# Performance work log

Hardware: AMD Instinct MI355X
Metric: run time of the kernel (lower is better)

## Reference

```python
import jax, jax.numpy as jnp
import numpy as np

N = 8192          # number of signals (rows of Y)
DIM_BASIS = 512   # signal dimension n
NUM_BASIS = 2048  # dictionary atoms m (overcomplete)
SC_ITERS = 20     # FISTA iterations
PM_ITERS = 100    # power-method iterations


def setup_inputs() -> dict:
    key = jax.random.key(0)
    kY, kW = jax.random.split(key)
    Y = jax.random.normal(kY, (N, DIM_BASIS), jnp.float32)
    W = jax.random.normal(kW, (DIM_BASIS, NUM_BASIS), jnp.float32)
    # NormDict applied in __init__: unit-norm columns
    W = W / jnp.linalg.norm(W, axis=0, keepdims=True)
    K = jnp.asarray(0.1, jnp.float32)  # lamda for FISTA soft-threshold
    return {"Y": Y, "W": W, "K": K}


def _soft(x, lam):
    return jnp.sign(x) * jax.nn.relu(jnp.abs(x) - lam)


def _power_method(W):
    # largest eigenvalue of W^T W (W: [n, m]); fixed random init for determinism
    X0 = jax.random.normal(jax.random.key(1), (1, W.shape[1]), W.dtype)

    def body(i, carry):
        X, _ = carry
        X = (X @ W.T) @ W          # X <- X W^T W, shape [1, m]
        nm = jnp.linalg.norm(X)
        return (X / nm, nm)

    _, nm = jax.lax.fori_loop(0, PM_ITERS, body, (X0, jnp.asarray(1.0, W.dtype)))
    return nm


def _fista(Y, W, lam, iters):
    c = _power_method(W)
    eta = 1.0 / c
    Gamma0 = _soft(Y @ (eta * W), lam)     # [N, m]
    Yn = jnp.linalg.norm(Y)

    def step(carry, _):
        Gamma, Z, t = carry
        residual = Z @ W.T - Y                              # [N, n]
        Gamma_new = _soft(Z - eta * (residual @ W), lam / c)
        t_new = (1.0 + jnp.sqrt(1.0 + 4.0 * t * t)) / 2.0
        Z_new = Gamma_new + ((t - 1.0) / t_new) * (Gamma_new - Gamma)
        nrm = jnp.linalg.norm(residual) / Yn
        return (Gamma_new, Z_new, t_new), nrm

    init = (Gamma0, Gamma0, jnp.asarray(1.0, Y.dtype))
    (Gamma, _, _), norms = jax.lax.scan(step, init, None, length=iters)
    return Gamma, norms


def reference(Y, W, K):
    # NormDict at start of forward (done on .data in torch -> no grad through norm)
    Wn = W / jax.lax.stop_gradient(jnp.linalg.norm(W, axis=0, keepdims=True))
    # W.requires_grad_(False) during sparse coding
    W_ng = jax.lax.stop_gradient(Wn)
    Gamma, norms = _fista(Y, W_ng, K, SC_ITERS)
    X = Gamma @ Wn.T   # reconstruction, grad flows to W here only
    return X, Gamma, norms
```

## Files before the change

### kernel.cpp

```cpp
#include <hip/hip_runtime.h>
#include <cmath>

#define NR   8192
#define DB   512
#define NB   2048
#define ITERS 20
#define NSQ   9

typedef _Float16 hfrag_t __attribute__((ext_vector_type(8)));
typedef __attribute__((ext_vector_type(4))) float accv_t;
typedef unsigned short us4 __attribute__((ext_vector_type(4)));
typedef unsigned short us8 __attribute__((ext_vector_type(8)));
typedef float f4 __attribute__((ext_vector_type(4)));

#define SL_Y2   0
#define SL_NUM  1
#define SL_DEN  2
#define SL_C    3
#define SL_ETA  4
#define SL_THR  5
#define SL_TR   6
#define SL_RES2 16

__device__ inline unsigned short f2h(float f) {
  _Float16 h = (_Float16)f;
  return __builtin_bit_cast(unsigned short, h);
}
__device__ inline float h2f(unsigned short u) {
  _Float16 h = __builtin_bit_cast(_Float16, u);
  return (float)h;
}
__device__ inline float softthr(float x, float t) {
  float a = fabsf(x) - t;
  return a > 0.f ? copysignf(a, x) : 0.f;
}


template<int MI, int NI, int NKT>
__device__ inline void gemm_tt(const unsigned short* __restrict__ At, int NTka,
                               const unsigned short* __restrict__ Bt, int NTkb,
                               int mt0, int nt0, accv_t acc[MI][NI]) {
  const int lane = threadIdx.x & 63;
  const int l16 = lane & 15, quad = lane >> 4;
  const int off = l16 * 16 + (quad & 1) * 8;
  const int kh = quad >> 1;
#pragma unroll
  for (int mi = 0; mi < MI; ++mi)
#pragma unroll
    for (int ni = 0; ni < NI; ++ni) acc[mi][ni] = (accv_t){0.f, 0.f, 0.f, 0.f};

#pragma unroll 4
  for (int kt = 0; kt < NKT; ++kt) {
    const int ktile = (kt << 1) + kh;
    hfrag_t af[MI], bf[NI];
#pragma unroll
    for (int mi = 0; mi < MI; ++mi)
      af[mi] = *(const hfrag_t*)&At[(((size_t)(mt0 + mi) * NTka + ktile) << 8) + off];
#pragma unroll
    for (int ni = 0; ni < NI; ++ni)
      bf[ni] = *(const hfrag_t*)&Bt[(((size_t)(nt0 + ni) * NTkb + ktile) << 8) + off];
#pragma unroll
    for (int mi = 0; mi < MI; ++mi)
#pragma unroll
      for (int ni = 0; ni < NI; ++ni)
        acc[mi][ni] = __builtin_amdgcn_mfma_f32_16x16x32_f16(bf[ni], af[mi], acc[mi][ni], 0, 0, 0);
  }
}

__device__ inline size_t ctile_off(int mt, int nt, int NTn) {
  int lane = threadIdx.x & 63;
  return (((size_t)mt * NTn + nt) << 8) + (lane & 15) * 16 + (lane >> 4) * 4;
}

__global__ void k_zero(float* slots, float* colsq) {
  if (threadIdx.x < 64) slots[threadIdx.x] = 0.f;
  for (int i = threadIdx.x; i < NB; i += 256) colsq[i] = 0.f;
}

__global__ void k_colsq(const float* __restrict__ W, float* __restrict__ colsq) {
  int j = blockIdx.x * 256 + threadIdx.x;
  int r0 = blockIdx.y * 64;
  float s = 0.f;
  for (int i = 0; i < 64; ++i) { float v = W[(size_t)(r0 + i) * NB + j]; s += v * v; }
  atomicAdd(&colsq[j], s);
}

__global__ void k_wnorm(const float* __restrict__ W, const float* __restrict__ colsq,
                        unsigned short* __restrict__ Wn_t, unsigned short* __restrict__ Wt_t) {
  int tx = threadIdx.x & 31, ty = threadIdx.x >> 5;
  int j = blockIdx.x * 32 + tx;
  float inv = 1.0f / sqrtf(colsq[j]);
#pragma unroll
  for (int r = 0; r < 4; ++r) {
    int i = blockIdx.y * 32 + ty + r * 8;
    unsigned short h = f2h(W[(size_t)i * NB + j] * inv);
    Wn_t[(((size_t)(i >> 4) * (NB / 16) + (j >> 4)) << 8) + (i & 15) * 16 + (j & 15)] = h;
    Wt_t[(((size_t)(j >> 4) * (DB / 16) + (i >> 4)) << 8) + (j & 15) * 16 + (i & 15)] = h;
  }
}

__global__ __launch_bounds__(256) void k_ynorm(const float* __restrict__ Y,
                                               unsigned short* __restrict__ Yh,
                                               float* __restrict__ slots) {
  __shared__ float part[4];
  int w = threadIdx.x >> 6, lane = threadIdx.x & 63;
  float s = 0.f;
#pragma unroll
  for (int rr = 0; rr < 4; ++rr) {
    int m = blockIdx.x * 16 + w * 4 + rr;
    const float* yrow = &Y[(size_t)m * DB + lane * 8];
    f4 v0 = *(const f4*)yrow;
    f4 v1 = *(const f4*)(yrow + 4);
    us8 h;
#pragma unroll
    for (int q = 0; q < 4; ++q) {
      h[q] = f2h(v0[q]);     s += v0[q] * v0[q];
      h[4 + q] = f2h(v1[q]); s += v1[q] * v1[q];
    }
    *(us8*)&Yh[(((size_t)(m >> 4) * 32 + (lane >> 1)) << 8) + (m & 15) * 16 + (lane & 1) * 8] = h;
  }
  for (int off = 32; off > 0; off >>= 1) s += __shfl_xor(s, off);
  if (lane == 0) part[w] = s;
  __syncthreads();
  if (threadIdx.x == 0) atomicAdd(&slots[SL_Y2], part[0] + part[1] + part[2] + part[3]);
}

__global__ __launch_bounds__(256) void k_sq(const float* __restrict__ S, float* __restrict__ D,
                                            const float* __restrict__ trIn, float* __restrict__ trOut) {
  __shared__ float tA[32][33], tB[32][33];
  int tx = threadIdx.x & 31, ty = threadIdx.x >> 5;
  int r0 = blockIdx.y * 32, c0 = blockIdx.x * 32;
  float inv = 1.0f / trIn[0];
  float acc[4] = {0.f, 0.f, 0.f, 0.f};
  for (int kt = 0; kt < 16; ++kt) {
    __syncthreads();
#pragma unroll
    for (int r = 0; r < 4; ++r) {
      tA[ty + r * 8][tx] = S[(size_t)(r0 + ty + r * 8) * DB + kt * 32 + tx];
      tB[ty + r * 8][tx] = S[(size_t)(kt * 32 + ty + r * 8) * DB + c0 + tx];
    }
    __syncthreads();
#pragma unroll
    for (int kk = 0; kk < 32; ++kk) {
      float b = tB[kk][tx];
#pragma unroll
      for (int r = 0; r < 4; ++r) acc[r] += tA[ty + r * 8][kk] * b;
    }
  }
  float inv2 = inv * inv;
#pragma unroll
  for (int r = 0; r < 4; ++r) {
    int row = r0 + ty + r * 8, col = c0 + tx;
    float v = acc[r] * inv2;
    D[(size_t)row * DB + col] = v;
    if (row == col) atomicAdd(trOut, v);
  }
}

__global__ void k_rayleigh(const float* __restrict__ Bm, const float* __restrict__ S,
                           float* __restrict__ slots) {
  int tid = blockIdx.x * 256 + threadIdx.x;
  float num = 0.f, den = 0.f;
  for (int i = tid; i < DB * DB; i += 256 * 256) {
    float s = S[i];
    num += Bm[i] * s;
    if ((i >> 9) == (i & 511)) den += s;
  }
  for (int off = 32; off > 0; off >>= 1) { num += __shfl_xor(num, off); den += __shfl_xor(den, off); }
  if ((threadIdx.x & 63) == 0) { atomicAdd(&slots[SL_NUM], num); atomicAdd(&slots[SL_DEN], den); }
}

__global__ void k_derive(float* slots, const float* __restrict__ Kp) {
  if (threadIdx.x == 0) {
    float cc = slots[SL_NUM] / slots[SL_DEN];
    slots[SL_C] = cc;
    float eta = 1.0f / cc;
    slots[SL_ETA] = eta;
    slots[SL_THR] = Kp[0] * eta;
  }
}

__global__ void k_norms(const float* __restrict__ slots, float* __restrict__ out) {
  int i = threadIdx.x;
  if (i < ITERS) out[i] = sqrtf(slots[SL_RES2 + i] / slots[SL_Y2]);
}

__global__ __launch_bounds__(512) void k_gemm_bbuild(const unsigned short* __restrict__ Wn_t,
                                                     float* __restrict__ Bm, float* __restrict__ slots) {
  __shared__ float red[4][64][33];
  accv_t acc[2][4];
  int w = threadIdx.x >> 6, lane = threadIdx.x & 63;
  int wk = w >> 2, wm = w & 3;
  int mt0 = blockIdx.y * 8 + wm * 2, nt0 = blockIdx.x * 4;
  const size_t koff = (size_t)wk * 64 * 256;
  gemm_tt<2, 4, NB / 64>(Wn_t + koff, NB / 16, Wn_t + koff, NB / 16, mt0, nt0, acc);
  if (wk == 1) {
#pragma unroll
    for (int mi = 0; mi < 2; ++mi)
#pragma unroll
      for (int ni = 0; ni < 4; ++ni)
#pragma unroll
        for (int r = 0; r < 4; ++r)
          red[wm][lane][mi * 16 + ni * 4 + r] = acc[mi][ni][r];
  }
  __syncthreads();
  if (wk == 0) {
    int l16 = lane & 15, quad = lane >> 4;
    float tr = 0.f;
#pragma unroll
    for (int mi = 0; mi < 2; ++mi)
#pragma unroll
      for (int ni = 0; ni < 4; ++ni) {
        int m = (mt0 + mi) * 16 + l16, nb = (nt0 + ni) * 16 + quad * 4;
        f4 o;
#pragma unroll
        for (int r = 0; r < 4; ++r) {
          o[r] = acc[mi][ni][r] + red[wm][lane][mi * 16 + ni * 4 + r];
          if (m == nb + r) tr += o[r];
        }
        *(f4*)&Bm[(size_t)m * DB + nb] = o;
      }
    if (tr != 0.f) atomicAdd(&slots[SL_TR], tr);
  }
}

__global__ __launch_bounds__(256) void k_gemm_init(const unsigned short* __restrict__ Yh,
                                                   const unsigned short* __restrict__ Wt_t,
                                                   const float* __restrict__ slots,
                                                   const float* __restrict__ Kp,
                                                   unsigned short* __restrict__ Gh,
                                                   unsigned short* __restrict__ Zh) {
  accv_t acc[4][4];
  int w = threadIdx.x >> 6;
  int h = blockIdx.x;
  int xcd = h & 7, slot = h >> 3;
  int band = xcd * 8 + (slot >> 4);
  int nt = slot & 15;
  int mt0 = band * 8 + (w >> 1) * 4, nt0 = nt * 8 + (w & 1) * 4;
  gemm_tt<4, 4, DB / 32>(Yh, DB / 16, Wt_t, DB / 16, mt0, nt0, acc);
  float eta = slots[SL_ETA], lam = Kp[0];
#pragma unroll
  for (int mi = 0; mi < 4; ++mi)
#pragma unroll
    for (int ni = 0; ni < 4; ++ni) {
      size_t tb = ctile_off(mt0 + mi, nt0 + ni, NB / 16);
      us4 gq;
#pragma unroll
      for (int r = 0; r < 4; ++r) gq[r] = f2h(softthr(acc[mi][ni][r] * eta, lam));
      *(us4*)&Gh[tb] = gq;
      *(us4*)&Zh[tb] = gq;
    }
}

__global__ __launch_bounds__(512) void k_gemm_res(const unsigned short* __restrict__ Zh,
                                                  const unsigned short* __restrict__ Wn_t,
                                                  const unsigned short* __restrict__ Yh,
                                                  unsigned short* __restrict__ Rh,
                                                  float* __restrict__ res2slot) {
  __shared__ float red[4][64][65];
  accv_t acc[4][4];
  int w = threadIdx.x >> 6, lane = threadIdx.x & 63;
  int wk = w >> 2, wm = w & 3;
  int h = blockIdx.x;
  int xcd = h & 7, slot = h >> 3;
  int band = xcd * 4 + (slot >> 3);
  int nt = slot & 7;
  int mt0 = band * 16 + wm * 4, nt0 = nt * 4;
  const size_t koff = (size_t)wk * 64 * 256;
  gemm_tt<4, 4, NB / 64>(Zh + koff, NB / 16, Wn_t + koff, NB / 16, mt0, nt0, acc);
  if (wk == 1) {
#pragma unroll
    for (int mi = 0; mi < 4; ++mi)
#pragma unroll
      for (int ni = 0; ni < 4; ++ni)
#pragma unroll
        for (int r = 0; r < 4; ++r)
          red[wm][lane][mi * 16 + ni * 4 + r] = acc[mi][ni][r];
  }
  __syncthreads();
  if (wk == 0) {
    float s2 = 0.f;
#pragma unroll
    for (int mi = 0; mi < 4; ++mi)
#pragma unroll
      for (int ni = 0; ni < 4; ++ni) {
        size_t tb = ctile_off(mt0 + mi, nt0 + ni, DB / 16);
        us4 yq = *(const us4*)&Yh[tb];
        us4 rq;
#pragma unroll
        for (int r = 0; r < 4; ++r) {
          float rv = acc[mi][ni][r] + red[wm][lane][mi * 16 + ni * 4 + r] - h2f(yq[r]);
          rq[r] = f2h(rv);
          s2 += rv * rv;
        }
        *(us4*)&Rh[tb] = rq;
      }
    for (int off = 32; off > 0; off >>= 1) s2 += __shfl_xor(s2, off);
    if (lane == 0) atomicAdd(res2slot, s2);
  }
}

__global__ __launch_bounds__(256) void k_gemm_upd(const unsigned short* __restrict__ Rh,
                                                  const unsigned short* __restrict__ Wt_t,
                                                  const float* __restrict__ slots,
                                                  unsigned short* __restrict__ Gh,
                                                  unsigned short* __restrict__ Zh,
                                                  float* __restrict__ GammaOut,
                                                  float mom, int writeFinal) {
  accv_t acc[4][4];
  int w = threadIdx.x >> 6, lane = threadIdx.x & 63;
  int h = blockIdx.x;
  int xcd = h & 7, slot = h >> 3;
  int band = xcd * 8 + (slot >> 4);
  int nt = slot & 15;
  int mt0 = band * 8 + (w >> 1) * 4, nt0 = nt * 8 + (w & 1) * 4;
  gemm_tt<4, 4, DB / 32>(Rh, DB / 16, Wt_t, DB / 16, mt0, nt0, acc);
  int l16 = lane & 15, quad = lane >> 4;
  float eta = slots[SL_ETA], thr = slots[SL_THR];
#pragma unroll
  for (int mi = 0; mi < 4; ++mi)
#pragma unroll
    for (int ni = 0; ni < 4; ++ni) {
      size_t tb = ctile_off(mt0 + mi, nt0 + ni, NB / 16);
      us4 zq = *(const us4*)&Zh[tb];
      us4 gq = *(const us4*)&Gh[tb];
      us4 gho, zho;
      f4 gf;
#pragma unroll
      for (int r = 0; r < 4; ++r) {
        float z = h2f(zq[r]);
        float gold = h2f(gq[r]);
        float gn = softthr(z - eta * acc[mi][ni][r], thr);
        float zn = gn + mom * (gn - gold);
        gho[r] = f2h(gn);
        zho[r] = f2h(zn);
        gf[r] = gn;
      }
      *(us4*)&Gh[tb] = gho;
      *(us4*)&Zh[tb] = zho;
      if (writeFinal) {
        int m = (mt0 + mi) * 16 + l16, nb = (nt0 + ni) * 16 + quad * 4;
        *(f4*)&GammaOut[(size_t)m * NB + nb] = gf;
      }
    }
}

__global__ __launch_bounds__(512) void k_gemm_x(const unsigned short* __restrict__ Gh,
                                                const unsigned short* __restrict__ Wn_t,
                                                float* __restrict__ X) {
  __shared__ float red[4][64][65];
  accv_t acc[4][4];
  int w = threadIdx.x >> 6, lane = threadIdx.x & 63;
  int wk = w >> 2, wm = w & 3;
  int h = blockIdx.x;
  int xcd = h & 7, slot = h >> 3;
  int band = xcd * 4 + (slot >> 3);
  int nt = slot & 7;
  int mt0 = band * 16 + wm * 4, nt0 = nt * 4;
  const size_t koff = (size_t)wk * 64 * 256;
  gemm_tt<4, 4, NB / 64>(Gh + koff, NB / 16, Wn_t + koff, NB / 16, mt0, nt0, acc);
  if (wk == 1) {
#pragma unroll
    for (int mi = 0; mi < 4; ++mi)
#pragma unroll
      for (int ni = 0; ni < 4; ++ni)
#pragma unroll
        for (int r = 0; r < 4; ++r)
          red[wm][lane][mi * 16 + ni * 4 + r] = acc[mi][ni][r];
  }
  __syncthreads();
  if (wk == 0) {
    int l16 = lane & 15, quad = lane >> 4;
#pragma unroll
    for (int mi = 0; mi < 4; ++mi)
#pragma unroll
      for (int ni = 0; ni < 4; ++ni) {
        int m = (mt0 + mi) * 16 + l16, nb = (nt0 + ni) * 16 + quad * 4;
        f4 o;
#pragma unroll
        for (int r = 0; r < 4; ++r)
          o[r] = acc[mi][ni][r] + red[wm][lane][mi * 16 + ni * 4 + r];
        *(f4*)&X[(size_t)m * DB + nb] = o;
      }
  }
}

extern "C" void kernel_launch(void* const* d_in, const int* in_sizes, int n_in,
                              void* d_out, int out_size, void* d_ws, size_t ws_size,
                              hipStream_t stream) {
  const float* Y  = (const float*)d_in[0];
  const float* W  = (const float*)d_in[1];
  const float* Kp = (const float*)d_in[2];

  float* Xout     = (float*)d_out;
  float* GammaOut = Xout + (size_t)NR * DB;
  float* NormsOut = GammaOut + (size_t)NR * NB;

  char* p = (char*)d_ws;
  auto carve = [&](size_t bytes) -> void* {
    void* r = (void*)p; p += (bytes + 255) & ~(size_t)255; return r;
  };
  float* slots = (float*)carve(64 * 4);
  float* colsq = (float*)carve(NB * 4);
  float* Bmat  = (float*)carve((size_t)DB * DB * 4);
  float* S0    = (float*)carve((size_t)DB * DB * 4);
  float* S1    = (float*)carve((size_t)DB * DB * 4);
  unsigned short* Wn_t = (unsigned short*)carve((size_t)DB * NB * 2);
  unsigned short* Wt_t = (unsigned short*)carve((size_t)NB * DB * 2);
  unsigned short* Yh   = (unsigned short*)carve((size_t)NR * DB * 2);
  unsigned short* Rh   = (unsigned short*)carve((size_t)NR * DB * 2);
  unsigned short* Zh   = (unsigned short*)carve((size_t)NR * NB * 2);
  unsigned short* Gh   = (unsigned short*)carve((size_t)NR * NB * 2);

  k_zero<<<1, 256, 0, stream>>>(slots, colsq);
  k_colsq<<<dim3(NB / 256, DB / 64), 256, 0, stream>>>(W, colsq);
  k_wnorm<<<dim3(NB / 32, DB / 32), 256, 0, stream>>>(W, colsq, Wn_t, Wt_t);
  k_ynorm<<<512, 256, 0, stream>>>(Y, Yh, slots);

  k_gemm_bbuild<<<dim3(DB / 64, DB / 128), 512, 0, stream>>>(Wn_t, Bmat, slots);
  float* ss[2] = {S0, S1};
  for (int k = 0; k < NSQ; ++k) {
    const float* in = (k == 0) ? Bmat : ss[(k + 1) & 1];
    k_sq<<<dim3(16, 16), 256, 0, stream>>>(in, ss[k & 1], slots + SL_TR + k, slots + SL_TR + k + 1);
  }
  k_rayleigh<<<256, 256, 0, stream>>>(Bmat, ss[(NSQ + 1) & 1], slots);
  k_derive<<<1, 64, 0, stream>>>(slots, Kp);

  k_gemm_init<<<1024, 256, 0, stream>>>(Yh, Wt_t, slots, Kp, Gh, Zh);
  double t = 1.0;
  for (int i = 0; i < ITERS; ++i) {
    k_gemm_res<<<256, 512, 0, stream>>>(Zh, Wn_t, Yh, Rh, slots + SL_RES2 + i);
    double tn = (1.0 + sqrt(1.0 + 4.0 * t * t)) / 2.0;
    float mom = (float)((t - 1.0) / tn);
    t = tn;
    k_gemm_upd<<<1024, 256, 0, stream>>>(Rh, Wt_t, slots, Gh, Zh, GammaOut,
                                         mom, (i == ITERS - 1) ? 1 : 0);
  }
  k_gemm_x<<<256, 512, 0, stream>>>(Gh, Wn_t, Xout);
  k_norms<<<1, 64, 0, stream>>>(slots, NormsOut);
}
```

Baseline: 2.148 ms.

## Split K across warp pairs in update GEMM with LDS reduction

The update GEMM (residual times W) now uses 512-thread blocks in which two groups of four warps each compute half of the K dimension for the same output tiles. The partial sums are exchanged through shared memory, and each warp finishes half of the M sub-tiles in the soft-threshold epilogue. Block tiling also changes, so each block covers a 16x4 tile region instead of 8x8. The aim is to double the number of waves working on each output and halve the serial K loop per warp, at the cost of an LDS reduction and a block-wide sync. Separately, the last iteration no longer writes Z, since it is not used after the loop.

```diff
diff --git a/kernel.cpp b/kernel.cpp
--- a/kernel.cpp
+++ b/kernel.cpp
@@ -300,46 +300,65 @@
   }
 }
 
-__global__ __launch_bounds__(256) void k_gemm_upd(const unsigned short* __restrict__ Rh,
+__global__ __launch_bounds__(512) void k_gemm_upd(const unsigned short* __restrict__ Rh,
                                                   const unsigned short* __restrict__ Wt_t,
                                                   const float* __restrict__ slots,
                                                   unsigned short* __restrict__ Gh,
                                                   unsigned short* __restrict__ Zh,
                                                   float* __restrict__ GammaOut,
                                                   float mom, int writeFinal) {
+  __shared__ float red[8][64][33];
   accv_t acc[4][4];
   int w = threadIdx.x >> 6, lane = threadIdx.x & 63;
+  int wk = w >> 2, wm = w & 3;
   int h = blockIdx.x;
   int xcd = h & 7, slot = h >> 3;
-  int band = xcd * 8 + (slot >> 4);
-  int nt = slot & 15;
-  int mt0 = band * 8 + (w >> 1) * 4, nt0 = nt * 8 + (w & 1) * 4;
-  gemm_tt<4, 4, DB / 32>(Rh, DB / 16, Wt_t, DB / 16, mt0, nt0, acc);
+  int band = xcd * 4 + (slot >> 5);
+  int nt = slot & 31;
+  int mt0 = band * 16 + wm * 4, nt0 = nt * 4;
+  const size_t koff = (size_t)wk * 16 * 256;
+  gemm_tt<4, 4, DB / 64>(Rh + koff, DB / 16, Wt_t + koff, DB / 16, mt0, nt0, acc);
+  {
+    int mbase = wk ? 0 : 2;
+#pragma unroll
+    for (int mi = 0; mi < 2; ++mi)
+#pragma unroll
+      for (int ni = 0; ni < 4; ++ni)
+#pragma unroll
+        for (int r = 0; r < 4; ++r)
+          red[w][lane][mi * 16 + ni * 4 + r] = acc[mbase + mi][ni][r];
+  }
+  __syncthreads();
+  const int fbase = wk ? 2 : 0;
+  const int pw = w ^ 4;
   int l16 = lane & 15, quad = lane >> 4;
   float eta = slots[SL_ETA], thr = slots[SL_THR];
 #pragma unroll
-  for (int mi = 0; mi < 4; ++mi)
+  for (int mi = 0; mi < 2; ++mi)
 #pragma unroll
     for (int ni = 0; ni < 4; ++ni) {
-      size_t tb = ctile_off(mt0 + mi, nt0 + ni, NB / 16);
+      int mt = fbase + mi;
+      size_t tb = ctile_off(mt0 + mt, nt0 + ni, NB / 16);
       us4 zq = *(const us4*)&Zh[tb];
       us4 gq = *(const us4*)&Gh[tb];
       us4 gho, zho;
       f4 gf;
 #pragma unroll
       for (int r = 0; r < 4; ++r) {
+        float g = acc[mt][ni][r] + red[pw][lane][mi * 16 + ni * 4 + r];
         float z = h2f(zq[r]);
         float gold = h2f(gq[r]);
-        float gn = softthr(z - eta * acc[mi][ni][r], thr);
+        float gn = softthr(z - eta * g, thr);
         float zn = gn + mom * (gn - gold);
         gho[r] = f2h(gn);
         zho[r] = f2h(zn);
         gf[r] = gn;
       }
       *(us4*)&Gh[tb] = gho;
-      *(us4*)&Zh[tb] = zho;
-      if (writeFinal) {
-        int m = (mt0 + mi) * 16 + l16, nb = (nt0 + ni) * 16 + quad * 4;
+      if (!writeFinal) {
+        *(us4*)&Zh[tb] = zho;
+      } else {
+        int m = (mt0 + mt) * 16 + l16, nb = (nt0 + ni) * 16 + quad * 4;
         *(f4*)&GammaOut[(size_t)m * NB + nb] = gf;
       }
     }
@@ -433,7 +452,7 @@
     double tn = (1.0 + sqrt(1.0 + 4.0 * t * t)) / 2.0;
     float mom = (float)((t - 1.0) / tn);
     t = tn;
-    k_gemm_upd<<<1024, 256, 0, stream>>>(Rh, Wt_t, slots, Gh, Zh, GammaOut,
+    k_gemm_upd<<<1024, 512, 0, stream>>>(Rh, Wt_t, slots, Gh, Zh, GammaOut,
                                          mom, (i == ITERS - 1) ? 1 : 0);
   }
   k_gemm_x<<<256, 512, 0, stream>>>(Gh, Wn_t, Xout);
```

Result: slower. 2.735 ms (+27.3%).
